# Kernel tuning notes

Hardware: AMD Instinct MI355X
Metric: run time of the kernel (lower is better)

Reference implementation:

```python
import jax, jax.numpy as jnp
import numpy as np
from math import sqrt

BLOCK_SIZE = 64
NUM_STEPS = 4


def _safe_normalize(x):
    n = jnp.linalg.norm(x, axis=-1, keepdims=True)
    safe_n = jnp.where(n > 0, n, 1.0)
    return jnp.where(n > 0, x / safe_n, x)


def _safe_inv_norm(x):
    n = jnp.linalg.norm(x, axis=-1, keepdims=True)
    safe_n = jnp.where(n > 0, n, 1.0)
    return jnp.where(n > 0, 1.0 / safe_n, 0.0)


def _project(x, u):
    # einsum('...i,...j,...j->...i', x, x, u)
    return x * jnp.sum(x * u, axis=-1, keepdims=True)


def _grad(lp, rp, Q, K):
    # lp: (b,h,j,l,k)  rp: (b,h,k,j,i)  Q: (b,h,l,j,v)  K: (b,h,k,i,v)
    ls = _safe_normalize(lp)
    rs = _safe_normalize(rp)
    left = ls ** 2
    right = rs ** 2
    # d_left
    r2 = jnp.sum(right ** 2, axis=-1)  # (b,h,k,j)
    KR = jnp.einsum('bhkji,bhkiv->bhkjv', right, K)
    t2l = jnp.einsum('bhkjv,bhljv->bhjlk', KR, Q)
    dl = jnp.einsum('bhkj,bhjlk->bhjlk', r2, left) - t2l
    dl = dl * 2 * ls
    dl = dl - _project(ls, dl)
    dl = dl * _safe_inv_norm(lp)
    # d_right
    l2 = jnp.sum(left ** 2, axis=-2)  # (b,h,j,k)
    LQ = jnp.einsum('bhjlk,bhljv->bhjkv', left, Q)
    t2r = jnp.einsum('bhjkv,bhkiv->bhkji', LQ, K)
    dr = jnp.einsum('bhjk,bhkji->bhkji', l2, right) - t2r
    dr = dr * 2 * rs
    dr = dr - _project(rs, dr)
    dr = dr * _safe_inv_norm(rp)
    return dl, dr


def _get_factors(query, key, attention_scale, step_size):
    B, H, S, D = query.shape
    bs = BLOCK_SIZE
    L = S // bs  # seq_len chosen divisible by block_size -> pad_amount = 0
    q = query / sqrt(D)
    q = q * jax.nn.softplus(attention_scale)[None, :, None, None]
    Q = q.reshape(B, H, L, bs, D)
    K = key.reshape(B, H, L, bs, D)
    lp = jnp.full((B, H, bs, L, L), 1.0 / sqrt(L), dtype=query.dtype)
    rp = jnp.full((B, H, L, bs, bs), 1.0 / sqrt(bs), dtype=query.dtype)
    for s in range(NUM_STEPS):
        dl, dr = _grad(lp, rp, Q, K)
        lp = lp - jax.nn.softplus(step_size[:, 0, s])[None, :, None, None, None] * dl
        rp = rp - jax.nn.softplus(step_size[:, 1, s])[None, :, None, None, None] * dr
    left = _safe_normalize(lp) ** 2
    right = _safe_normalize(rp) ** 2
    return left, right


def setup_inputs() -> dict:
    key = jax.random.key(0)
    ks = jax.random.split(key, 5)
    B, H, S, D = 4, 12, 2048, 64
    return {
        'query': jax.random.normal(ks[0], (B, H, S, D), dtype=jnp.float32),
        'key': jax.random.normal(ks[1], (B, H, S, D), dtype=jnp.float32),
        'value': jax.random.normal(ks[2], (B, H, S, D), dtype=jnp.float32),
        'attention_scale': jax.random.normal(ks[3], (H,), dtype=jnp.float32),
        'step_size': jax.random.normal(ks[4], (H, 2, NUM_STEPS), dtype=jnp.float32),
    }


def reference(query, key, value, attention_scale, step_size):
    B, H, S, D = query.shape
    bs = BLOCK_SIZE
    L = S // bs
    left, right = _get_factors(query, key, attention_scale, step_size)
    X = value.reshape(B, H, L, bs, D)
    Y = jnp.einsum('bhkji,bhkiv->bhkjv', right, X)
    Z = jnp.einsum('bhjlk,bhkjv->bhljv', left, Y)
    return Z.reshape(B, H, S, D)
```

## Files before the change

kernel.cpp:

```cpp
#include <hip/hip_runtime.h>
#include <cmath>

#define BH_ 48
#define NH_ 12
#define SS_ 2048

__device__ __forceinline__ float softplus_f(float x) {
    return fmaxf(x, 0.0f) + log1pf(expf(-fabsf(x)));
}


__global__ __launch_bounds__(64) void kA0(const float* __restrict__ key,
                                          float* __restrict__ mean) {
    int blk = blockIdx.x; int bh = blk >> 5; int k = blk & 31;
    int t = threadIdx.x;
    const float* kb = key + ((size_t)bh * SS_ + k * 64) * 64;
    float acc = 0.f;
    #pragma unroll
    for (int i = 0; i < 64; ++i) acc += kb[i * 64 + t];
    mean[((size_t)bh * 32 + k) * 64 + t] = acc * (1.0f / 64.0f);
}

template <int STEP>
__global__ __launch_bounds__(256) void kB(const float* __restrict__ query,
                                          const float* __restrict__ attn_scale,
                                          const float* __restrict__ step_size,
                                          float* __restrict__ lp,
                                          const float* __restrict__ KR,
                                          const float* __restrict__ r2,
                                          float* __restrict__ LQ,
                                          float* __restrict__ l2) {
    int blk = blockIdx.x; int bh = blk >> 6; int j = blk & 63;
    int h = bh % NH_; int t = threadIdx.x;
    __shared__ float Qs[32][68];
    __shared__ float KRs[32][68];
    __shared__ float leS[32][33];
    __shared__ float t2S[32][33];

    float qscale = softplus_f(attn_scale[h]) * 0.125f;
    float sp0 = softplus_f(step_size[h * 8 + STEP]);

    for (int idx = t; idx < 512; idx += 256) {
        int r = idx >> 4, c4 = (idx & 15) * 4;
        float4 q = *(const float4*)&query[((size_t)bh * SS_ + r * 64 + j) * 64 + c4];
        q.x *= qscale; q.y *= qscale; q.z *= qscale; q.w *= qscale;
        *(float4*)&Qs[r][c4] = q;
        float4 kr;
        if (STEP == 0) kr = *(const float4*)&KR[((size_t)bh * 32 + r) * 64 + c4];
        else           kr = *(const float4*)&KR[((size_t)(bh * 32 + r) * 64 + j) * 64 + c4];
        *(float4*)&KRs[r][c4] = kr;
    }

    int lo = t >> 3, c0 = (t & 7) * 4;
    float lpv[4], r2v[4];
    if (STEP == 0) {
        #pragma unroll
        for (int d = 0; d < 4; ++d) { lpv[d] = 0.17677669529663687f; r2v[d] = 1.0f / 64.0f; }
    } else {
        float4 v = *(const float4*)&lp[((size_t)(bh * 64 + j)) * 1024 + lo * 32 + c0];
        lpv[0] = v.x; lpv[1] = v.y; lpv[2] = v.z; lpv[3] = v.w;
        float4 w = *(const float4*)&r2[((size_t)(bh * 64 + j)) * 32 + c0];
        r2v[0] = w.x; r2v[1] = w.y; r2v[2] = w.z; r2v[3] = w.w;
    }
    float s = lpv[0]*lpv[0] + lpv[1]*lpv[1] + lpv[2]*lpv[2] + lpv[3]*lpv[3];
    s += __shfl_xor(s, 1); s += __shfl_xor(s, 2); s += __shfl_xor(s, 4);
    float n = sqrtf(s);
    float invn = (n > 0.f) ? 1.0f / n : 0.f;
    float ls[4], le[4];
    #pragma unroll
    for (int d = 0; d < 4; ++d) {
        ls[d] = lpv[d] * invn; le[d] = ls[d] * ls[d];
        leS[lo][c0 + d] = le[d];
    }
    __syncthreads();

    {
        int ml = t >> 4, mk = t & 15;
        float a00 = 0, a01 = 0, a10 = 0, a11 = 0;
        #pragma unroll 4
        for (int v4 = 0; v4 < 16; ++v4) {
            float4 q0 = *(const float4*)&Qs[ml][v4 * 4];
            float4 q1 = *(const float4*)&Qs[ml + 16][v4 * 4];
            float4 r0 = *(const float4*)&KRs[mk][v4 * 4];
            float4 r1 = *(const float4*)&KRs[mk + 16][v4 * 4];
            a00 += q0.x*r0.x + q0.y*r0.y + q0.z*r0.z + q0.w*r0.w;
            a01 += q0.x*r1.x + q0.y*r1.y + q0.z*r1.z + q0.w*r1.w;
            a10 += q1.x*r0.x + q1.y*r0.y + q1.z*r0.z + q1.w*r0.w;
            a11 += q1.x*r1.x + q1.y*r1.y + q1.z*r1.z + q1.w*r1.w;
        }
        t2S[ml][mk] = a00; t2S[ml][mk + 16] = a01;
        t2S[ml + 16][mk] = a10; t2S[ml + 16][mk + 16] = a11;
    }
    __syncthreads();

    {
        float dl[4]; float rd = 0.f;
        #pragma unroll
        for (int d = 0; d < 4; ++d) {
            float t2 = t2S[lo][c0 + d];
            dl[d] = 2.f * ls[d] * (r2v[d] * le[d] - t2);
            rd += ls[d] * dl[d];
        }
        rd += __shfl_xor(rd, 1); rd += __shfl_xor(rd, 2); rd += __shfl_xor(rd, 4);
        float4 outv;
        outv.x = lpv[0] - sp0 * ((dl[0] - ls[0] * rd) * invn);
        outv.y = lpv[1] - sp0 * ((dl[1] - ls[1] * rd) * invn);
        outv.z = lpv[2] - sp0 * ((dl[2] - ls[2] * rd) * invn);
        outv.w = lpv[3] - sp0 * ((dl[3] - ls[3] * rd) * invn);
        *(float4*)&lp[((size_t)(bh * 64 + j)) * 1024 + lo * 32 + c0] = outv;
    }

    {
        int mk = t >> 4, v0 = (t & 15) * 4;
        float4 b0 = {0, 0, 0, 0}, b1 = {0, 0, 0, 0};
        #pragma unroll 4
        for (int l = 0; l < 32; ++l) {
            float e0 = leS[l][mk], e1 = leS[l][mk + 16];
            float4 q = *(const float4*)&Qs[l][v0];
            b0.x += e0 * q.x; b0.y += e0 * q.y; b0.z += e0 * q.z; b0.w += e0 * q.w;
            b1.x += e1 * q.x; b1.y += e1 * q.y; b1.z += e1 * q.z; b1.w += e1 * q.w;
        }
        float* LQj = LQ + ((size_t)(bh * 64 + j)) * 2048;
        *(float4*)&LQj[mk * 64 + v0] = b0;
        *(float4*)&LQj[(mk + 16) * 64 + v0] = b1;
    }

    if (t < 64) {
        int k = t & 31, hh = t >> 5;
        float s2 = 0.f;
        #pragma unroll
        for (int l = hh * 16; l < hh * 16 + 16; ++l) { float x = leS[l][k]; s2 += x * x; }
        s2 += __shfl_xor(s2, 32);
        if (hh == 0) l2[(bh * 32 + k) * 64 + j] = s2;
    }
}

template <int STEP>
__global__ __launch_bounds__(256) void kCA(const float* __restrict__ key,
                                           const float* __restrict__ value,
                                           const float* __restrict__ step_size,
                                           float* __restrict__ rp,
                                           const float* __restrict__ LQ,
                                           const float* __restrict__ l2,
                                           float* __restrict__ KR,
                                           float* __restrict__ r2) {
    int blk = blockIdx.x; int bh = blk >> 5; int k = blk & 31;
    int h = bh % NH_; int t = threadIdx.x;
    __shared__ float kS[64][68];
    __shared__ float lqS[64][68];
    __shared__ float l2S[64];

    float sp1 = softplus_f(step_size[h * 8 + 4 + STEP]);
    float* rpk = rp + ((size_t)(bh * 32 + k)) * 4096;

    for (int idx = t; idx < 1024; idx += 256) {
        int r = idx >> 4, c4 = (idx & 15) * 4;
        *(float4*)&kS[r][c4]  = *(const float4*)&key[((size_t)bh * SS_ + k * 64 + r) * 64 + c4];
        *(float4*)&lqS[r][c4] = *(const float4*)&LQ[((size_t)(bh * 64 + r) * 32 + k) * 64 + c4];
    }
    if (t < 64) l2S[t] = l2[(bh * 32 + k) * 64 + t];

    int jo = t >> 2, c0 = (t & 3) * 16;
    float rv[16];
    if (STEP == 0) {
        #pragma unroll
        for (int i = 0; i < 16; ++i) rv[i] = 0.125f;
    } else {
        #pragma unroll
        for (int q4 = 0; q4 < 4; ++q4) {
            float4 v = *(const float4*)&rpk[jo * 64 + c0 + q4 * 4];
            rv[q4 * 4] = v.x; rv[q4 * 4 + 1] = v.y; rv[q4 * 4 + 2] = v.z; rv[q4 * 4 + 3] = v.w;
        }
    }
    float s2 = 0.f;
    #pragma unroll
    for (int i = 0; i < 16; ++i) s2 += rv[i] * rv[i];
    s2 += __shfl_xor(s2, 1); s2 += __shfl_xor(s2, 2);
    float n = sqrtf(s2);
    float invn = (n > 0.f) ? 1.0f / n : 0.f;
    __syncthreads();

    int mi = t & 15, mj = t >> 4;
    float acc[4][4] = {};
    #pragma unroll 2
    for (int v4 = 0; v4 < 16; ++v4) {
        float4 lq[4], kk[4];
        #pragma unroll
        for (int d = 0; d < 4; ++d) lq[d] = *(const float4*)&lqS[mj + 16 * d][v4 * 4];
        #pragma unroll
        for (int d = 0; d < 4; ++d) kk[d] = *(const float4*)&kS[mi + 16 * d][v4 * 4];
        #pragma unroll
        for (int a = 0; a < 4; ++a)
            #pragma unroll
            for (int b = 0; b < 4; ++b)
                acc[a][b] += lq[a].x * kk[b].x + lq[a].y * kk[b].y +
                             lq[a].z * kk[b].z + lq[a].w * kk[b].w;
    }
    __syncthreads();
    #pragma unroll
    for (int a = 0; a < 4; ++a)
        #pragma unroll
        for (int b = 0; b < 4; ++b) lqS[mj + 16 * a][mi + 16 * b] = acc[a][b];
    if (STEP == 3) {
        for (int idx = t; idx < 1024; idx += 256) {
            int r = idx >> 4, c4 = (idx & 15) * 4;
            *(float4*)&kS[r][c4] = *(const float4*)&value[((size_t)bh * SS_ + k * 64 + r) * 64 + c4];
        }
    }
    __syncthreads();

    float dv[16];
    #pragma unroll
    for (int q4 = 0; q4 < 4; ++q4) {
        float4 v = *(const float4*)&lqS[jo][c0 + q4 * 4];
        dv[q4 * 4] = v.x; dv[q4 * 4 + 1] = v.y; dv[q4 * 4 + 2] = v.z; dv[q4 * 4 + 3] = v.w;
    }
    float l2j = l2S[jo];
    float dot = 0.f;
    #pragma unroll
    for (int i = 0; i < 16; ++i) {
        float rs = rv[i] * invn;
        dv[i] = 2.f * rs * (l2j * rs * rs - dv[i]);
        dot += rs * dv[i];
    }
    dot += __shfl_xor(dot, 1); dot += __shfl_xor(dot, 2);
    float s2n = 0.f, s4n = 0.f;
    #pragma unroll
    for (int i = 0; i < 16; ++i) {
        float rs = rv[i] * invn;
        float d = (dv[i] - rs * dot) * invn;
        rv[i] -= sp1 * d;
        float x2 = rv[i] * rv[i];
        s2n += x2; s4n += x2 * x2;
    }
    s2n += __shfl_xor(s2n, 1); s2n += __shfl_xor(s2n, 2);
    s4n += __shfl_xor(s4n, 1); s4n += __shfl_xor(s4n, 2);
    float nn = sqrtf(s2n);
    float inn = (nn > 0.f) ? 1.0f / nn : 0.f;
    if (STEP < 3) {
        #pragma unroll
        for (int q4 = 0; q4 < 4; ++q4) {
            float4 v = make_float4(rv[q4*4], rv[q4*4+1], rv[q4*4+2], rv[q4*4+3]);
            *(float4*)&rpk[jo * 64 + c0 + q4 * 4] = v;
        }
        if ((t & 3) == 0) {
            float i2 = inn * inn;
            r2[(bh * 64 + jo) * 32 + k] = i2 * i2 * s4n;
        }
    }
    __syncthreads();

    #pragma unroll
    for (int q4 = 0; q4 < 4; ++q4) {
        float4 w;
        float a0 = rv[q4*4] * inn, a1 = rv[q4*4+1] * inn, a2 = rv[q4*4+2] * inn, a3 = rv[q4*4+3] * inn;
        w.x = a0 * a0; w.y = a1 * a1; w.z = a2 * a2; w.w = a3 * a3;
        *(float4*)&lqS[jo][c0 + q4 * 4] = w;
    }
    __syncthreads();

    {
        float4 oc[4] = {{0,0,0,0}, {0,0,0,0}, {0,0,0,0}, {0,0,0,0}};
        int v0 = mi * 4;
        #pragma unroll 2
        for (int i4 = 0; i4 < 16; ++i4) {
            float4 k0 = *(const float4*)&kS[i4 * 4 + 0][v0];
            float4 k1 = *(const float4*)&kS[i4 * 4 + 1][v0];
            float4 k2 = *(const float4*)&kS[i4 * 4 + 2][v0];
            float4 k3 = *(const float4*)&kS[i4 * 4 + 3][v0];
            #pragma unroll
            for (int a = 0; a < 4; ++a) {
                float4 rg = *(const float4*)&lqS[mj + 16 * a][i4 * 4];
                oc[a].x += rg.x * k0.x + rg.y * k1.x + rg.z * k2.x + rg.w * k3.x;
                oc[a].y += rg.x * k0.y + rg.y * k1.y + rg.z * k2.y + rg.w * k3.y;
                oc[a].z += rg.x * k0.z + rg.y * k1.z + rg.z * k2.z + rg.w * k3.z;
                oc[a].w += rg.x * k0.w + rg.y * k1.w + rg.z * k2.w + rg.w * k3.w;
            }
        }
        float* KRk = KR + ((size_t)(bh * 32 + k)) * 4096;
        #pragma unroll
        for (int a = 0; a < 4; ++a)
            *(float4*)&KRk[(mj + 16 * a) * 64 + v0] = oc[a];
    }
}

__global__ __launch_bounds__(256) void kZ(const float* __restrict__ lp,
                                          const float* Y,
                                          float* out) {
    int blk = blockIdx.x; int bh = blk >> 6; int j = blk & 63;
    int t = threadIdx.x;
    __shared__ float Ys[32][68];
    __shared__ float leS[32][33];

    for (int idx = t; idx < 512; idx += 256) {
        int r = idx >> 4, c4 = (idx & 15) * 4;
        *(float4*)&Ys[r][c4] = *(const float4*)&Y[((size_t)(bh * 32 + r) * 64 + j) * 64 + c4];
    }
    int lo = t >> 3, c0 = (t & 7) * 4;
    float4 v = *(const float4*)&lp[((size_t)(bh * 64 + j)) * 1024 + lo * 32 + c0];
    float s = v.x*v.x + v.y*v.y + v.z*v.z + v.w*v.w;
    s += __shfl_xor(s, 1); s += __shfl_xor(s, 2); s += __shfl_xor(s, 4);
    float n = sqrtf(s);
    float invn = (n > 0.f) ? 1.0f / n : 0.f;
    float a0 = v.x * invn, a1 = v.y * invn, a2 = v.z * invn, a3 = v.w * invn;
    leS[lo][c0] = a0 * a0; leS[lo][c0 + 1] = a1 * a1;
    leS[lo][c0 + 2] = a2 * a2; leS[lo][c0 + 3] = a3 * a3;
    __syncthreads();

    {
        int ml = t >> 4, v0 = (t & 15) * 4;
        float4 b0 = {0, 0, 0, 0}, b1 = {0, 0, 0, 0};
        #pragma unroll 4
        for (int kk = 0; kk < 32; ++kk) {
            float e0 = leS[ml][kk], e1 = leS[ml + 16][kk];
            float4 y = *(const float4*)&Ys[kk][v0];
            b0.x += e0 * y.x; b0.y += e0 * y.y; b0.z += e0 * y.z; b0.w += e0 * y.w;
            b1.x += e1 * y.x; b1.y += e1 * y.y; b1.z += e1 * y.z; b1.w += e1 * y.w;
        }
        *(float4*)&out[((size_t)bh * SS_ + ml * 64 + j) * 64 + v0] = b0;
        *(float4*)&out[((size_t)bh * SS_ + (ml + 16) * 64 + j) * 64 + v0] = b1;
    }
}

extern "C" void kernel_launch(void* const* d_in, const int* in_sizes, int n_in,
                              void* d_out, int out_size, void* d_ws, size_t ws_size,
                              hipStream_t stream) {
    const float* query = (const float*)d_in[0];
    const float* key   = (const float*)d_in[1];
    const float* value = (const float*)d_in[2];
    const float* attn  = (const float*)d_in[3];
    const float* ss    = (const float*)d_in[4];
    float* out = (float*)d_out;

    const size_t n_lp = (size_t)BH_ * 64 * 32 * 32;
    const size_t n_rp = (size_t)BH_ * 32 * 64 * 64;
    const size_t n_LQ = (size_t)BH_ * 64 * 32 * 64;
    const size_t n_r2 = (size_t)BH_ * 64 * 32;
    const size_t n_l2 = (size_t)BH_ * 32 * 64;
    const size_t need = (n_lp + n_rp + n_LQ + n_r2 + n_l2) * sizeof(float);
    if (ws_size < need) return;

    float* ws = (float*)d_ws;
    float* lp = ws;
    float* rp = lp + n_lp;
    float* LQ = rp + n_rp;
    float* r2 = LQ + n_LQ;
    float* l2 = r2 + n_r2;
    float* KR = out;
    float* mean = r2;

    dim3 blkD(256);
    const int gK = BH_ * 32;
    const int gJ = BH_ * 64;

    kA0<<<gK, dim3(64), 0, stream>>>(key, mean);
    kB<0><<<gJ, blkD, 0, stream>>>(query, attn, ss, lp, mean, r2, LQ, l2);
    kCA<0><<<gK, blkD, 0, stream>>>(key, value, ss, rp, LQ, l2, KR, r2);
    kB<1><<<gJ, blkD, 0, stream>>>(query, attn, ss, lp, KR, r2, LQ, l2);
    kCA<1><<<gK, blkD, 0, stream>>>(key, value, ss, rp, LQ, l2, KR, r2);
    kB<2><<<gJ, blkD, 0, stream>>>(query, attn, ss, lp, KR, r2, LQ, l2);
    kCA<2><<<gK, blkD, 0, stream>>>(key, value, ss, rp, LQ, l2, KR, r2);
    kB<3><<<gJ, blkD, 0, stream>>>(query, attn, ss, lp, KR, r2, LQ, l2);
    kCA<3><<<gK, blkD, 0, stream>>>(key, value, ss, rp, LQ, l2, KR, r2);
    kZ<<<gJ, blkD, 0, stream>>>(lp, KR, out);
}
```

Before: 376.9 us.

## Shrink blocks to one wavefront and give each thread larger register tiles

All kernels now run with 64 threads per block, a single wavefront, instead of 256. Each thread computes a bigger register tile: 4x4 in kB, 8x8 in kCA's LQ·K product, and whole 64-wide rows of rp. This raises arithmetic intensity per LDS load and removes cross-wavefront barriers and shuffles. The cost is much higher register pressure, especially rv[64] plus acc[8][8] in kCA, which may spill or cut occupancy. Fewer waves per block also leave less latency hiding for the global loads.

```diff
diff --git a/kernel.cpp b/kernel.cpp
--- a/kernel.cpp
+++ b/kernel.cpp
@@ -22,25 +22,25 @@
 }
 
 template <int STEP>
-__global__ __launch_bounds__(256) void kB(const float* __restrict__ query,
-                                          const float* __restrict__ attn_scale,
-                                          const float* __restrict__ step_size,
-                                          float* __restrict__ lp,
-                                          const float* __restrict__ KR,
-                                          const float* __restrict__ r2,
-                                          float* __restrict__ LQ,
-                                          float* __restrict__ l2) {
+__global__ __launch_bounds__(64) void kB(const float* __restrict__ query,
+                                         const float* __restrict__ attn_scale,
+                                         const float* __restrict__ step_size,
+                                         float* __restrict__ lp,
+                                         const float* __restrict__ KR,
+                                         const float* __restrict__ r2,
+                                         float* __restrict__ LQ,
+                                         float* __restrict__ l2) {
     int blk = blockIdx.x; int bh = blk >> 6; int j = blk & 63;
     int h = bh % NH_; int t = threadIdx.x;
     __shared__ float Qs[32][68];
     __shared__ float KRs[32][68];
-    __shared__ float leS[32][33];
-    __shared__ float t2S[32][33];
+    __shared__ float leS[32][36];
+    __shared__ float t2S[32][36];
 
     float qscale = softplus_f(attn_scale[h]) * 0.125f;
     float sp0 = softplus_f(step_size[h * 8 + STEP]);
 
-    for (int idx = t; idx < 512; idx += 256) {
+    for (int idx = t; idx < 512; idx += 64) {
         int r = idx >> 4, c4 = (idx & 15) * 4;
         float4 q = *(const float4*)&query[((size_t)bh * SS_ + r * 64 + j) * 64 + c4];
         q.x *= qscale; q.y *= qscale; q.z *= qscale; q.w *= qscale;
@@ -51,99 +51,127 @@
         *(float4*)&KRs[r][c4] = kr;
     }
 
-    int lo = t >> 3, c0 = (t & 7) * 4;
-    float lpv[4], r2v[4];
+    int lo = t >> 1, c0 = (t & 1) * 16;
+    float* lpj = lp + ((size_t)(bh * 64 + j)) * 1024;
+    float lpv[16], r2v[16];
     if (STEP == 0) {
         #pragma unroll
-        for (int d = 0; d < 4; ++d) { lpv[d] = 0.17677669529663687f; r2v[d] = 1.0f / 64.0f; }
+        for (int d = 0; d < 16; ++d) { lpv[d] = 0.17677669529663687f; r2v[d] = 1.0f / 64.0f; }
     } else {
-        float4 v = *(const float4*)&lp[((size_t)(bh * 64 + j)) * 1024 + lo * 32 + c0];
-        lpv[0] = v.x; lpv[1] = v.y; lpv[2] = v.z; lpv[3] = v.w;
-        float4 w = *(const float4*)&r2[((size_t)(bh * 64 + j)) * 32 + c0];
-        r2v[0] = w.x; r2v[1] = w.y; r2v[2] = w.z; r2v[3] = w.w;
-    }
-    float s = lpv[0]*lpv[0] + lpv[1]*lpv[1] + lpv[2]*lpv[2] + lpv[3]*lpv[3];
-    s += __shfl_xor(s, 1); s += __shfl_xor(s, 2); s += __shfl_xor(s, 4);
+        #pragma unroll
+        for (int q4 = 0; q4 < 4; ++q4) {
+            float4 v = *(const float4*)&lpj[lo * 32 + c0 + q4 * 4];
+            lpv[q4*4] = v.x; lpv[q4*4+1] = v.y; lpv[q4*4+2] = v.z; lpv[q4*4+3] = v.w;
+            float4 w = *(const float4*)&r2[((size_t)(bh * 64 + j)) * 32 + c0 + q4 * 4];
+            r2v[q4*4] = w.x; r2v[q4*4+1] = w.y; r2v[q4*4+2] = w.z; r2v[q4*4+3] = w.w;
+        }
+    }
+    float s = 0.f;
+    #pragma unroll
+    for (int d = 0; d < 16; ++d) s += lpv[d] * lpv[d];
+    s += __shfl_xor(s, 1);
     float n = sqrtf(s);
     float invn = (n > 0.f) ? 1.0f / n : 0.f;
-    float ls[4], le[4];
-    #pragma unroll
-    for (int d = 0; d < 4; ++d) {
-        ls[d] = lpv[d] * invn; le[d] = ls[d] * ls[d];
-        leS[lo][c0 + d] = le[d];
-    }
-    __syncthreads();
-
-    {
-        int ml = t >> 4, mk = t & 15;
-        float a00 = 0, a01 = 0, a10 = 0, a11 = 0;
-        #pragma unroll 4
+    float ls[16], le[16];
+    #pragma unroll
+    for (int d = 0; d < 16; ++d) { ls[d] = lpv[d] * invn; le[d] = ls[d] * ls[d]; }
+    #pragma unroll
+    for (int q4 = 0; q4 < 4; ++q4)
+        *(float4*)&leS[lo][c0 + q4 * 4] = make_float4(le[q4*4], le[q4*4+1], le[q4*4+2], le[q4*4+3]);
+    __syncthreads();
+
+    {
+        int rg = t >> 3, cg = t & 7;
+        float acc[4][4] = {};
+        #pragma unroll 2
         for (int v4 = 0; v4 < 16; ++v4) {
-            float4 q0 = *(const float4*)&Qs[ml][v4 * 4];
-            float4 q1 = *(const float4*)&Qs[ml + 16][v4 * 4];
-            float4 r0 = *(const float4*)&KRs[mk][v4 * 4];
-            float4 r1 = *(const float4*)&KRs[mk + 16][v4 * 4];
-            a00 += q0.x*r0.x + q0.y*r0.y + q0.z*r0.z + q0.w*r0.w;
-            a01 += q0.x*r1.x + q0.y*r1.y + q0.z*r1.z + q0.w*r1.w;
-            a10 += q1.x*r0.x + q1.y*r0.y + q1.z*r0.z + q1.w*r0.w;
-            a11 += q1.x*r1.x + q1.y*r1.y + q1.z*r1.z + q1.w*r1.w;
-        }
-        t2S[ml][mk] = a00; t2S[ml][mk + 16] = a01;
-        t2S[ml + 16][mk] = a10; t2S[ml + 16][mk + 16] = a11;
-    }
-    __syncthreads();
-
-    {
-        float dl[4]; float rd = 0.f;
-        #pragma unroll
-        for (int d = 0; d < 4; ++d) {
-            float t2 = t2S[lo][c0 + d];
-            dl[d] = 2.f * ls[d] * (r2v[d] * le[d] - t2);
-            rd += ls[d] * dl[d];
-        }
-        rd += __shfl_xor(rd, 1); rd += __shfl_xor(rd, 2); rd += __shfl_xor(rd, 4);
-        float4 outv;
-        outv.x = lpv[0] - sp0 * ((dl[0] - ls[0] * rd) * invn);
-        outv.y = lpv[1] - sp0 * ((dl[1] - ls[1] * rd) * invn);
-        outv.z = lpv[2] - sp0 * ((dl[2] - ls[2] * rd) * invn);
-        outv.w = lpv[3] - sp0 * ((dl[3] - ls[3] * rd) * invn);
-        *(float4*)&lp[((size_t)(bh * 64 + j)) * 1024 + lo * 32 + c0] = outv;
-    }
-
-    {
-        int mk = t >> 4, v0 = (t & 15) * 4;
-        float4 b0 = {0, 0, 0, 0}, b1 = {0, 0, 0, 0};
-        #pragma unroll 4
-        for (int l = 0; l < 32; ++l) {
-            float e0 = leS[l][mk], e1 = leS[l][mk + 16];
-            float4 q = *(const float4*)&Qs[l][v0];
-            b0.x += e0 * q.x; b0.y += e0 * q.y; b0.z += e0 * q.z; b0.w += e0 * q.w;
-            b1.x += e1 * q.x; b1.y += e1 * q.y; b1.z += e1 * q.z; b1.w += e1 * q.w;
+            float4 qv[4], rv4[4];
+            #pragma unroll
+            for (int d = 0; d < 4; ++d) qv[d]  = *(const float4*)&Qs[rg + 8*d][v4*4];
+            #pragma unroll
+            for (int d = 0; d < 4; ++d) rv4[d] = *(const float4*)&KRs[cg + 8*d][v4*4];
+            #pragma unroll
+            for (int a = 0; a < 4; ++a)
+                #pragma unroll
+                for (int b = 0; b < 4; ++b)
+                    acc[a][b] += qv[a].x*rv4[b].x + qv[a].y*rv4[b].y +
+                                 qv[a].z*rv4[b].z + qv[a].w*rv4[b].w;
+        }
+        #pragma unroll
+        for (int a = 0; a < 4; ++a)
+            #pragma unroll
+            for (int b = 0; b < 4; ++b) t2S[rg + 8*a][cg + 8*b] = acc[a][b];
+    }
+    __syncthreads();
+
+    {
+        float dl[16]; float rd = 0.f;
+        #pragma unroll
+        for (int q4 = 0; q4 < 4; ++q4) {
+            float4 t2 = *(const float4*)&t2S[lo][c0 + q4 * 4];
+            float tv[4] = {t2.x, t2.y, t2.z, t2.w};
+            #pragma unroll
+            for (int d = 0; d < 4; ++d) {
+                int i = q4*4 + d;
+                dl[i] = 2.f * ls[i] * (r2v[i] * le[i] - tv[d]);
+                rd += ls[i] * dl[i];
+            }
+        }
+        rd += __shfl_xor(rd, 1);
+        #pragma unroll
+        for (int q4 = 0; q4 < 4; ++q4) {
+            float o0 = lpv[q4*4]   - sp0 * ((dl[q4*4]   - ls[q4*4]   * rd) * invn);
+            float o1 = lpv[q4*4+1] - sp0 * ((dl[q4*4+1] - ls[q4*4+1] * rd) * invn);
+            float o2 = lpv[q4*4+2] - sp0 * ((dl[q4*4+2] - ls[q4*4+2] * rd) * invn);
+            float o3 = lpv[q4*4+3] - sp0 * ((dl[q4*4+3] - ls[q4*4+3] * rd) * invn);
+            *(float4*)&lpj[lo * 32 + c0 + q4 * 4] = make_float4(o0, o1, o2, o3);
+        }
+    }
+
+    {
+        int rg = t >> 3, v0 = (t & 7) * 4;
+        float4 b0[4] = {{0,0,0,0},{0,0,0,0},{0,0,0,0},{0,0,0,0}};
+        float4 b1[4] = {{0,0,0,0},{0,0,0,0},{0,0,0,0},{0,0,0,0}};
+        #pragma unroll 2
+        for (int l4 = 0; l4 < 8; ++l4) {
+            #pragma unroll
+            for (int dl = 0; dl < 4; ++dl) {
+                int l = l4 * 4 + dl;
+                float4 q0 = *(const float4*)&Qs[l][v0];
+                float4 q1 = *(const float4*)&Qs[l][v0 + 32];
+                #pragma unroll
+                for (int a = 0; a < 4; ++a) {
+                    float e = leS[l][rg + 8*a];
+                    b0[a].x += e*q0.x; b0[a].y += e*q0.y; b0[a].z += e*q0.z; b0[a].w += e*q0.w;
+                    b1[a].x += e*q1.x; b1[a].y += e*q1.y; b1[a].z += e*q1.z; b1[a].w += e*q1.w;
+                }
+            }
         }
         float* LQj = LQ + ((size_t)(bh * 64 + j)) * 2048;
-        *(float4*)&LQj[mk * 64 + v0] = b0;
-        *(float4*)&LQj[(mk + 16) * 64 + v0] = b1;
-    }
-
-    if (t < 64) {
-        int k = t & 31, hh = t >> 5;
+        #pragma unroll
+        for (int a = 0; a < 4; ++a) {
+            *(float4*)&LQj[(rg + 8*a) * 64 + v0] = b0[a];
+            *(float4*)&LQj[(rg + 8*a) * 64 + v0 + 32] = b1[a];
+        }
+    }
+
+    if (t < 32) {
         float s2 = 0.f;
         #pragma unroll
-        for (int l = hh * 16; l < hh * 16 + 16; ++l) { float x = leS[l][k]; s2 += x * x; }
-        s2 += __shfl_xor(s2, 32);
-        if (hh == 0) l2[(bh * 32 + k) * 64 + j] = s2;
+        for (int l = 0; l < 32; ++l) { float x = leS[l][t]; s2 += x * x; }
+        l2[(bh * 32 + t) * 64 + j] = s2;
     }
 }
 
 template <int STEP>
-__global__ __launch_bounds__(256) void kCA(const float* __restrict__ key,
-                                           const float* __restrict__ value,
-                                           const float* __restrict__ step_size,
-                                           float* __restrict__ rp,
-                                           const float* __restrict__ LQ,
-                                           const float* __restrict__ l2,
-                                           float* __restrict__ KR,
-                                           float* __restrict__ r2) {
+__global__ __launch_bounds__(64) void kCA(const float* __restrict__ key,
+                                          const float* __restrict__ value,
+                                          const float* __restrict__ step_size,
+                                          float* __restrict__ rp,
+                                          const float* __restrict__ LQ,
+                                          const float* __restrict__ l2,
+                                          float* __restrict__ KR,
+                                          float* __restrict__ r2) {
     int blk = blockIdx.x; int bh = blk >> 5; int k = blk & 31;
     int h = bh % NH_; int t = threadIdx.x;
     __shared__ float kS[64][68];
@@ -153,172 +181,194 @@
     float sp1 = softplus_f(step_size[h * 8 + 4 + STEP]);
     float* rpk = rp + ((size_t)(bh * 32 + k)) * 4096;
 
-    for (int idx = t; idx < 1024; idx += 256) {
+    for (int idx = t; idx < 1024; idx += 64) {
         int r = idx >> 4, c4 = (idx & 15) * 4;
         *(float4*)&kS[r][c4]  = *(const float4*)&key[((size_t)bh * SS_ + k * 64 + r) * 64 + c4];
         *(float4*)&lqS[r][c4] = *(const float4*)&LQ[((size_t)(bh * 64 + r) * 32 + k) * 64 + c4];
     }
-    if (t < 64) l2S[t] = l2[(bh * 32 + k) * 64 + t];
-
-    int jo = t >> 2, c0 = (t & 3) * 16;
-    float rv[16];
+    l2S[t] = l2[(bh * 32 + k) * 64 + t];
+    __syncthreads();
+
+    int tj = t >> 3, ti = t & 7;
+    {
+        float acc[8][8] = {};
+        #pragma unroll 2
+        for (int v4 = 0; v4 < 16; ++v4) {
+            float4 lq[8], kk[8];
+            #pragma unroll
+            for (int d = 0; d < 8; ++d) lq[d] = *(const float4*)&lqS[tj + 8*d][v4*4];
+            #pragma unroll
+            for (int d = 0; d < 8; ++d) kk[d] = *(const float4*)&kS[ti + 8*d][v4*4];
+            #pragma unroll
+            for (int a = 0; a < 8; ++a)
+                #pragma unroll
+                for (int b = 0; b < 8; ++b)
+                    acc[a][b] += lq[a].x*kk[b].x + lq[a].y*kk[b].y +
+                                 lq[a].z*kk[b].z + lq[a].w*kk[b].w;
+        }
+        __syncthreads();
+        #pragma unroll
+        for (int a = 0; a < 8; ++a)
+            #pragma unroll
+            for (int b = 0; b < 8; ++b) lqS[tj + 8*a][ti + 8*b] = acc[a][b];
+    }
+    if (STEP == 3) {
+        for (int idx = t; idx < 1024; idx += 64) {
+            int r = idx >> 4, c4 = (idx & 15) * 4;
+            *(float4*)&kS[r][c4] = *(const float4*)&value[((size_t)bh * SS_ + k * 64 + r) * 64 + c4];
+        }
+    }
+    __syncthreads();
+
+    float rv[64];
     if (STEP == 0) {
         #pragma unroll
-        for (int i = 0; i < 16; ++i) rv[i] = 0.125f;
+        for (int i = 0; i < 64; ++i) rv[i] = 0.125f;
     } else {
         #pragma unroll
-        for (int q4 = 0; q4 < 4; ++q4) {
-            float4 v = *(const float4*)&rpk[jo * 64 + c0 + q4 * 4];
-            rv[q4 * 4] = v.x; rv[q4 * 4 + 1] = v.y; rv[q4 * 4 + 2] = v.z; rv[q4 * 4 + 3] = v.w;
+        for (int q4 = 0; q4 < 16; ++q4) {
+            float4 v = *(const float4*)&rpk[t * 64 + q4 * 4];
+            rv[q4*4] = v.x; rv[q4*4+1] = v.y; rv[q4*4+2] = v.z; rv[q4*4+3] = v.w;
         }
     }
     float s2 = 0.f;
     #pragma unroll
-    for (int i = 0; i < 16; ++i) s2 += rv[i] * rv[i];
-    s2 += __shfl_xor(s2, 1); s2 += __shfl_xor(s2, 2);
+    for (int i = 0; i < 64; ++i) s2 += rv[i] * rv[i];
     float n = sqrtf(s2);
     float invn = (n > 0.f) ? 1.0f / n : 0.f;
-    __syncthreads();
-
-    int mi = t & 15, mj = t >> 4;
-    float acc[4][4] = {};
-    #pragma unroll 2
-    for (int v4 = 0; v4 < 16; ++v4) {
-        float4 lq[4], kk[4];
-        #pragma unroll
-        for (int d = 0; d < 4; ++d) lq[d] = *(const float4*)&lqS[mj + 16 * d][v4 * 4];
-        #pragma unroll
-        for (int d = 0; d < 4; ++d) kk[d] = *(const float4*)&kS[mi + 16 * d][v4 * 4];
-        #pragma unroll
-        for (int a = 0; a < 4; ++a)
-            #pragma unroll
-            for (int b = 0; b < 4; ++b)
-                acc[a][b] += lq[a].x * kk[b].x + lq[a].y * kk[b].y +
-                             lq[a].z * kk[b].z + lq[a].w * kk[b].w;
-    }
-    __syncthreads();
-    #pragma unroll
-    for (int a = 0; a < 4; ++a)
-        #pragma unroll
-        for (int b = 0; b < 4; ++b) lqS[mj + 16 * a][mi + 16 * b] = acc[a][b];
-    if (STEP == 3) {
-        for (int idx = t; idx < 1024; idx += 256) {
-            int r = idx >> 4, c4 = (idx & 15) * 4;
-            *(float4*)&kS[r][c4] = *(const float4*)&value[((size_t)bh * SS_ + k * 64 + r) * 64 + c4];
-        }
-    }
-    __syncthreads();
-
-    float dv[16];
-    #pragma unroll
-    for (int q4 = 0; q4 < 4; ++q4) {
-        float4 v = *(const float4*)&lqS[jo][c0 + q4 * 4];
-        dv[q4 * 4] = v.x; dv[q4 * 4 + 1] = v.y; dv[q4 * 4 + 2] = v.z; dv[q4 * 4 + 3] = v.w;
-    }
-    float l2j = l2S[jo];
+    float l2j = l2S[t];
     float dot = 0.f;
     #pragma unroll
-    for (int i = 0; i < 16; ++i) {
-        float rs = rv[i] * invn;
-        dv[i] = 2.f * rs * (l2j * rs * rs - dv[i]);
-        dot += rs * dv[i];
-    }
-    dot += __shfl_xor(dot, 1); dot += __shfl_xor(dot, 2);
+    for (int q4 = 0; q4 < 16; ++q4) {
+        float4 tv = *(const float4*)&lqS[t][q4 * 4];
+        float rs0 = rv[q4*4]   * invn; float d0 = 2.f*rs0*(l2j*rs0*rs0 - tv.x); dot += rs0*d0;
+        float rs1 = rv[q4*4+1] * invn; float d1 = 2.f*rs1*(l2j*rs1*rs1 - tv.y); dot += rs1*d1;
+        float rs2 = rv[q4*4+2] * invn; float d2 = 2.f*rs2*(l2j*rs2*rs2 - tv.z); dot += rs2*d2;
+        float rs3 = rv[q4*4+3] * invn; float d3 = 2.f*rs3*(l2j*rs3*rs3 - tv.w); dot += rs3*d3;
+        *(float4*)&lqS[t][q4 * 4] = make_float4(d0, d1, d2, d3);
+    }
     float s2n = 0.f, s4n = 0.f;
     #pragma unroll
-    for (int i = 0; i < 16; ++i) {
-        float rs = rv[i] * invn;
-        float d = (dv[i] - rs * dot) * invn;
-        rv[i] -= sp1 * d;
-        float x2 = rv[i] * rv[i];
-        s2n += x2; s4n += x2 * x2;
-    }
-    s2n += __shfl_xor(s2n, 1); s2n += __shfl_xor(s2n, 2);
-    s4n += __shfl_xor(s4n, 1); s4n += __shfl_xor(s4n, 2);
+    for (int q4 = 0; q4 < 16; ++q4) {
+        float4 dv4 = *(const float4*)&lqS[t][q4 * 4];
+        float dvv[4] = {dv4.x, dv4.y, dv4.z, dv4.w};
+        #pragma unroll
+        for (int d = 0; d < 4; ++d) {
+            int i = q4*4 + d;
+            float rs = rv[i] * invn;
+            float dd = (dvv[d] - rs * dot) * invn;
+            rv[i] -= sp1 * dd;
+            float x2 = rv[i] * rv[i];
+            s2n += x2; s4n += x2 * x2;
+        }
+    }
     float nn = sqrtf(s2n);
     float inn = (nn > 0.f) ? 1.0f / nn : 0.f;
     if (STEP < 3) {
         #pragma unroll
-        for (int q4 = 0; q4 < 4; ++q4) {
-            float4 v = make_float4(rv[q4*4], rv[q4*4+1], rv[q4*4+2], rv[q4*4+3]);
-            *(float4*)&rpk[jo * 64 + c0 + q4 * 4] = v;
-        }
-        if ((t & 3) == 0) {
-            float i2 = inn * inn;
-            r2[(bh * 64 + jo) * 32 + k] = i2 * i2 * s4n;
-        }
-    }
-    __syncthreads();
-
-    #pragma unroll
-    for (int q4 = 0; q4 < 4; ++q4) {
-        float4 w;
-        float a0 = rv[q4*4] * inn, a1 = rv[q4*4+1] * inn, a2 = rv[q4*4+2] * inn, a3 = rv[q4*4+3] * inn;
-        w.x = a0 * a0; w.y = a1 * a1; w.z = a2 * a2; w.w = a3 * a3;
-        *(float4*)&lqS[jo][c0 + q4 * 4] = w;
-    }
-    __syncthreads();
-
-    {
-        float4 oc[4] = {{0,0,0,0}, {0,0,0,0}, {0,0,0,0}, {0,0,0,0}};
-        int v0 = mi * 4;
+        for (int q4 = 0; q4 < 16; ++q4)
+            *(float4*)&rpk[t * 64 + q4 * 4] =
+                make_float4(rv[q4*4], rv[q4*4+1], rv[q4*4+2], rv[q4*4+3]);
+        float i2 = inn * inn;
+        r2[(bh * 64 + t) * 32 + k] = i2 * i2 * s4n;
+    }
+    #pragma unroll
+    for (int q4 = 0; q4 < 16; ++q4) {
+        float a0 = rv[q4*4]*inn, a1 = rv[q4*4+1]*inn, a2 = rv[q4*4+2]*inn, a3 = rv[q4*4+3]*inn;
+        *(float4*)&lqS[t][q4 * 4] = make_float4(a0*a0, a1*a1, a2*a2, a3*a3);
+    }
+    __syncthreads();
+
+    {
+        float4 oc0[8] = {{0,0,0,0},{0,0,0,0},{0,0,0,0},{0,0,0,0},
+                         {0,0,0,0},{0,0,0,0},{0,0,0,0},{0,0,0,0}};
+        float4 oc1[8] = {{0,0,0,0},{0,0,0,0},{0,0,0,0},{0,0,0,0},
+                         {0,0,0,0},{0,0,0,0},{0,0,0,0},{0,0,0,0}};
+        int v0 = ti * 4;
         #pragma unroll 2
         for (int i4 = 0; i4 < 16; ++i4) {
-            float4 k0 = *(const float4*)&kS[i4 * 4 + 0][v0];
-            float4 k1 = *(const float4*)&kS[i4 * 4 + 1][v0];
-            float4 k2 = *(const float4*)&kS[i4 * 4 + 2][v0];
-            float4 k3 = *(const float4*)&kS[i4 * 4 + 3][v0];
-            #pragma unroll
-            for (int a = 0; a < 4; ++a) {
-                float4 rg = *(const float4*)&lqS[mj + 16 * a][i4 * 4];
-                oc[a].x += rg.x * k0.x + rg.y * k1.x + rg.z * k2.x + rg.w * k3.x;
-                oc[a].y += rg.x * k0.y + rg.y * k1.y + rg.z * k2.y + rg.w * k3.y;
-                oc[a].z += rg.x * k0.z + rg.y * k1.z + rg.z * k2.z + rg.w * k3.z;
-                oc[a].w += rg.x * k0.w + rg.y * k1.w + rg.z * k2.w + rg.w * k3.w;
+            float4 rg[8];
+            #pragma unroll
+            for (int d = 0; d < 8; ++d) rg[d] = *(const float4*)&lqS[tj + 8*d][i4*4];
+            #pragma unroll
+            for (int di = 0; di < 4; ++di) {
+                float4 ka = *(const float4*)&kS[i4*4 + di][v0];
+                float4 kb = *(const float4*)&kS[i4*4 + di][v0 + 32];
+                #pragma unroll
+                for (int a = 0; a < 8; ++a) {
+                    float r = (di == 0) ? rg[a].x : (di == 1) ? rg[a].y :
+                              (di == 2) ? rg[a].z : rg[a].w;
+                    oc0[a].x += r*ka.x; oc0[a].y += r*ka.y; oc0[a].z += r*ka.z; oc0[a].w += r*ka.w;
+                    oc1[a].x += r*kb.x; oc1[a].y += r*kb.y; oc1[a].z += r*kb.z; oc1[a].w += r*kb.w;
+                }
             }
         }
         float* KRk = KR + ((size_t)(bh * 32 + k)) * 4096;
         #pragma unroll
-        for (int a = 0; a < 4; ++a)
-            *(float4*)&KRk[(mj + 16 * a) * 64 + v0] = oc[a];
-    }
-}
-
-__global__ __launch_bounds__(256) void kZ(const float* __restrict__ lp,
-                                          const float* Y,
-                                          float* out) {
+        for (int a = 0; a < 8; ++a) {
+            *(float4*)&KRk[(tj + 8*a) * 64 + v0] = oc0[a];
+            *(float4*)&KRk[(tj + 8*a) * 64 + v0 + 32] = oc1[a];
+        }
+    }
+}
+
+__global__ __launch_bounds__(64) void kZ(const float* __restrict__ lp,
+                                         const float* Y,
+                                         float* out) {
     int blk = blockIdx.x; int bh = blk >> 6; int j = blk & 63;
     int t = threadIdx.x;
     __shared__ float Ys[32][68];
-    __shared__ float leS[32][33];
-
-    for (int idx = t; idx < 512; idx += 256) {
+    __shared__ float leS[32][36];
+
+    for (int idx = t; idx < 512; idx += 64) {
         int r = idx >> 4, c4 = (idx & 15) * 4;
         *(float4*)&Ys[r][c4] = *(const float4*)&Y[((size_t)(bh * 32 + r) * 64 + j) * 64 + c4];
     }
-    int lo = t >> 3, c0 = (t & 7) * 4;
-    float4 v = *(const float4*)&lp[((size_t)(bh * 64 + j)) * 1024 + lo * 32 + c0];
-    float s = v.x*v.x + v.y*v.y + v.z*v.z + v.w*v.w;
-    s += __shfl_xor(s, 1); s += __shfl_xor(s, 2); s += __shfl_xor(s, 4);
+    int lo = t >> 1, c0 = (t & 1) * 16;
+    const float* lpj = lp + ((size_t)(bh * 64 + j)) * 1024;
+    float lpv[16];
+    #pragma unroll
+    for (int q4 = 0; q4 < 4; ++q4) {
+        float4 v = *(const float4*)&lpj[lo * 32 + c0 + q4 * 4];
+        lpv[q4*4] = v.x; lpv[q4*4+1] = v.y; lpv[q4*4+2] = v.z; lpv[q4*4+3] = v.w;
+    }
+    float s = 0.f;
+    #pragma unroll
+    for (int d = 0; d < 16; ++d) s += lpv[d] * lpv[d];
+    s += __shfl_xor(s, 1);
     float n = sqrtf(s);
     float invn = (n > 0.f) ? 1.0f / n : 0.f;
-    float a0 = v.x * invn, a1 = v.y * invn, a2 = v.z * invn, a3 = v.w * invn;
-    leS[lo][c0] = a0 * a0; leS[lo][c0 + 1] = a1 * a1;
-    leS[lo][c0 + 2] = a2 * a2; leS[lo][c0 + 3] = a3 * a3;
-    __syncthreads();
-
-    {
-        int ml = t >> 4, v0 = (t & 15) * 4;
-        float4 b0 = {0, 0, 0, 0}, b1 = {0, 0, 0, 0};
-        #pragma unroll 4
-        for (int kk = 0; kk < 32; ++kk) {
-            float e0 = leS[ml][kk], e1 = leS[ml + 16][kk];
-            float4 y = *(const float4*)&Ys[kk][v0];
-            b0.x += e0 * y.x; b0.y += e0 * y.y; b0.z += e0 * y.z; b0.w += e0 * y.w;
-            b1.x += e1 * y.x; b1.y += e1 * y.y; b1.z += e1 * y.z; b1.w += e1 * y.w;
-        }
-        *(float4*)&out[((size_t)bh * SS_ + ml * 64 + j) * 64 + v0] = b0;
-        *(float4*)&out[((size_t)bh * SS_ + (ml + 16) * 64 + j) * 64 + v0] = b1;
+    #pragma unroll
+    for (int q4 = 0; q4 < 4; ++q4) {
+        float a0 = lpv[q4*4]*invn, a1 = lpv[q4*4+1]*invn, a2 = lpv[q4*4+2]*invn, a3 = lpv[q4*4+3]*invn;
+        *(float4*)&leS[lo][c0 + q4 * 4] = make_float4(a0*a0, a1*a1, a2*a2, a3*a3);
+    }
+    __syncthreads();
+
+    {
+        int rg = t >> 3, v0 = (t & 7) * 4;
+        float4 b0[4] = {{0,0,0,0},{0,0,0,0},{0,0,0,0},{0,0,0,0}};
+        float4 b1[4] = {{0,0,0,0},{0,0,0,0},{0,0,0,0},{0,0,0,0}};
+        #pragma unroll 2
+        for (int k4 = 0; k4 < 8; ++k4) {
+            #pragma unroll
+            for (int dk = 0; dk < 4; ++dk) {
+                int kk = k4 * 4 + dk;
+                float4 y0 = *(const float4*)&Ys[kk][v0];
+                float4 y1 = *(const float4*)&Ys[kk][v0 + 32];
+                #pragma unroll
+                for (int a = 0; a < 4; ++a) {
+                    float e = leS[rg + 8*a][kk];
+                    b0[a].x += e*y0.x; b0[a].y += e*y0.y; b0[a].z += e*y0.z; b0[a].w += e*y0.w;
+                    b1[a].x += e*y1.x; b1[a].y += e*y1.y; b1[a].z += e*y1.z; b1[a].w += e*y1.w;
+                }
+            }
+        }
+        #pragma unroll
+        for (int a = 0; a < 4; ++a) {
+            *(float4*)&out[((size_t)bh * SS_ + (rg + 8*a) * 64 + j) * 64 + v0] = b0[a];
+            *(float4*)&out[((size_t)bh * SS_ + (rg + 8*a) * 64 + j) * 64 + v0 + 32] = b1[a];
+        }
     }
 }
 
@@ -349,11 +399,11 @@
     float* KR = out;
     float* mean = r2;
 
-    dim3 blkD(256);
+    dim3 blkD(64);
     const int gK = BH_ * 32;
     const int gJ = BH_ * 64;
 
-    kA0<<<gK, dim3(64), 0, stream>>>(key, mean);
+    kA0<<<gK, blkD, 0, stream>>>(key, mean);
     kB<0><<<gJ, blkD, 0, stream>>>(query, attn, ss, lp, mean, r2, LQ, l2);
     kCA<0><<<gK, blkD, 0, stream>>>(key, value, ss, rp, LQ, l2, KR, r2);
     kB<1><<<gJ, blkD, 0, stream>>>(query, attn, ss, lp, KR, r2, LQ, l2);
```

Result: slower. 485.2 us (+28.7%).
